# Optimization experiments

Hardware: AMD Instinct MI355X
Metric: run time of the kernel (lower is better)

Reference implementation:

```python
import math
import jax, jax.numpy as jnp
import numpy as np

NUM_HEADS, RAD_PTS, LVL_PTS = 8, 4, 1
P = RAD_PTS * LVL_PTS


def setup_inputs() -> dict:
    B, Nq, Din = 2, 21760, 256
    hw = np.array([[128, 128], [64, 64], [32, 32], [16, 16]], np.int64)
    sizes = hw[:, 0] * hw[:, 1]
    offs = np.concatenate([[0], np.cumsum(sizes)[:-1]]).astype(np.int64)
    Ns = int(sizes.sum())
    map_ids = np.tile(np.repeat(np.arange(4), sizes)[None], (B, 1)).astype(np.int64)

    key = jax.random.key(0)
    ks = jax.random.split(key, 8)
    in_feats = jax.random.normal(ks[0], (B, Nq, Din), jnp.float32)
    sample_feats = jax.random.normal(ks[1], (B, Ns, Din), jnp.float32)
    sample_priors = jax.random.uniform(ks[2], (B, Nq, 2), jnp.float32)

    # sample_offsets bias: radial grid init as in the torch module
    thetas = np.arange(NUM_HEADS) * (2.0 * math.pi / NUM_HEADS)
    grid = np.stack([np.cos(thetas), np.sin(thetas), np.zeros(NUM_HEADS)], 1)
    grid = grid / np.abs(grid).max(1, keepdims=True)
    grid = np.tile(grid.reshape(NUM_HEADS, 1, 1, 3), (1, RAD_PTS, LVL_PTS, 1))
    grid = grid * np.arange(1, RAD_PTS + 1).reshape(1, RAD_PTS, 1, 1)
    bo = jnp.asarray(grid.reshape(-1), jnp.float32)

    Wo = jax.random.normal(ks[3], (NUM_HEADS * P * 3, Din), jnp.float32) * 0.01
    Wa = jax.random.normal(ks[4], (NUM_HEADS * P, Din), jnp.float32) * 0.01
    ba = jnp.zeros((NUM_HEADS * P,), jnp.float32)
    s = 1.0 / np.sqrt(Din)
    Wv = jax.random.normal(ks[5], (Din, Din), jnp.float32) * s
    bv = jnp.zeros((Din,), jnp.float32)
    Wout = jax.random.normal(ks[6], (Din, Din), jnp.float32) * s
    bout = jnp.zeros((Din,), jnp.float32)

    return dict(in_feats=in_feats, sample_priors=sample_priors, sample_feats=sample_feats,
                map_hw=jnp.asarray(hw), map_offs=jnp.asarray(offs), map_ids=jnp.asarray(map_ids),
                Wo=Wo, bo=bo, Wa=Wa, ba=ba, Wv=Wv, bv=bv, Wout=Wout, bout=bout)


def _trilinear_sample(val, map_hw, map_offs, xy, z, L):
    # val [B,Ns,H,D]; xy [B,Q,H,P,2] normalized; z [B,Q,H,P] in ~[0,1]
    B, Ns, H, D = val.shape
    Q = xy.shape[1]
    val_t = val.transpose(0, 2, 1, 3)  # [B,H,Ns,D]
    x, y = xy[..., 0], xy[..., 1]
    lvl_f = z * (L - 1)
    l0 = jnp.floor(lvl_f).astype(jnp.int32)
    wz = lvl_f - l0.astype(lvl_f.dtype)

    def gather(idx):  # idx [B,Q,H,P] int32 -> [B,Q,H,P,D]
        it = idx.transpose(0, 2, 1, 3).reshape(B, H, Q * P, 1)
        g = jnp.take_along_axis(val_t, it, axis=2)  # [B,H,Q*P,D]
        return g.reshape(B, H, Q, P, D).transpose(0, 2, 1, 3, 4)

    def sample_level(lvl):  # bilinear sample within pyramid level `lvl` (zero padding)
        valid_l = (lvl >= 0) & (lvl < L)
        lc = jnp.clip(lvl, 0, L - 1)
        Hl = map_hw[lc, 0].astype(jnp.int32)
        Wl = map_hw[lc, 1].astype(jnp.int32)
        off = map_offs[lc].astype(jnp.int32)
        xf = x * Wl.astype(x.dtype) - 0.5
        yf = y * Hl.astype(x.dtype) - 0.5
        x0 = jnp.floor(xf).astype(jnp.int32)
        y0 = jnp.floor(yf).astype(jnp.int32)
        dx = xf - x0.astype(x.dtype)
        dy = yf - y0.astype(x.dtype)
        out = jnp.zeros((B, Q, H, P, D), x.dtype)
        corners = [(x0, y0, (1 - dx) * (1 - dy)), (x0 + 1, y0, dx * (1 - dy)),
                   (x0, y0 + 1, (1 - dx) * dy), (x0 + 1, y0 + 1, dx * dy)]
        for xi, yi, w in corners:
            ok = valid_l & (xi >= 0) & (xi < Wl) & (yi >= 0) & (yi < Hl)
            idx = off + jnp.clip(yi, 0, Hl - 1) * Wl + jnp.clip(xi, 0, Wl - 1)
            out = out + gather(idx) * (w * ok.astype(x.dtype))[..., None]
        return out

    return sample_level(l0) * (1 - wz)[..., None] + sample_level(l0 + 1) * wz[..., None]


def reference(in_feats, sample_priors, sample_feats, map_hw, map_offs, map_ids,
              Wo, bo, Wa, ba, Wv, bv, Wout, bout):
    B, Nq, _ = in_feats.shape
    Ns = sample_feats.shape[1]
    L = map_hw.shape[0]
    D = Wv.shape[0] // NUM_HEADS

    val = (sample_feats @ Wv.T + bv).reshape(B, Ns, NUM_HEADS, D)
    offs = (in_feats @ Wo.T + bo).reshape(B, Nq, NUM_HEADS, P, 3)

    # sample_priors last dim == 2: normalize offsets by (W, H) of the query's map
    norm = map_hw[:, ::-1][map_ids].astype(offs.dtype)  # [B,Nq,2] (w,h)
    sample_xy = sample_priors[:, :, None, None, :2] + offs[..., :2] / norm[:, :, None, None, :]

    lvl_off = jnp.arange(LVL_PTS, dtype=offs.dtype) - 0.5 * (LVL_PTS - 1)
    z_grid = map_ids[:, :, None, None, None].astype(offs.dtype) + lvl_off  # [B,Nq,1,1,Lp]
    z_grid = jnp.broadcast_to(z_grid, (B, Nq, NUM_HEADS, RAD_PTS, LVL_PTS)).reshape(B, Nq, NUM_HEADS, P)
    sample_z = (z_grid + jnp.tanh(offs[..., 2])) / (L - 1)

    attn = jax.nn.softmax((in_feats @ Wa.T + ba).reshape(B, Nq, NUM_HEADS, P), axis=3)

    sampled = _trilinear_sample(val, map_hw, map_offs, sample_xy, sample_z, L)  # [B,Nq,H,P,D]
    attn_feats = jnp.einsum('bqhpd,bqhp->bqhd', sampled, attn).reshape(B, Nq, NUM_HEADS * D)
    return attn_feats @ Wout.T + bout
```

## Files before the change

### kernel.cpp

```cpp
#include <hip/hip_runtime.h>
#include <hip/hip_bf16.h>
#include <math.h>

typedef __bf16 bf16x8 __attribute__((ext_vector_type(8)));
typedef float f32x4 __attribute__((ext_vector_type(4)));
typedef unsigned short ushort8 __attribute__((ext_vector_type(8)));

static __device__ __forceinline__ unsigned short f2bf(float f) {
    union { float f; unsigned u; } c; c.f = f;
    unsigned r = c.u + 0x7FFFu + ((c.u >> 16) & 1u);
    return (unsigned short)(r >> 16);
}
static __device__ __forceinline__ float bf2f(unsigned short u) {
    union { unsigned u; float f; } c; c.u = ((unsigned)u) << 16;
    return c.f;
}

__global__ __launch_bounds__(256) void convert_weights(
    const float* __restrict__ Wv, const float* __restrict__ Wo,
    const float* __restrict__ Wa, const float* __restrict__ Wout,
    const float* __restrict__ bo, const float* __restrict__ ba,
    unsigned short* __restrict__ Wv_b, unsigned short* __restrict__ Woa_b,
    unsigned short* __restrict__ Wout_b, float* __restrict__ boa)
{
    int gid = blockIdx.x * blockDim.x + threadIdx.x;
    int stride = gridDim.x * blockDim.x;
    for (int i = gid; i < 163840; i += stride) {
        if (i < 65536)       Wv_b[i] = f2bf(Wv[i]);
        else if (i < 90112)  Woa_b[i - 65536] = f2bf(Wo[i - 65536]);
        else if (i < 98304)  Woa_b[i - 65536] = f2bf(Wa[i - 90112]);
        else                 Wout_b[i - 98304] = f2bf(Wout[i - 98304]);
    }
    if (gid < 96)       boa[gid] = bo[gid];
    else if (gid < 128) boa[gid] = ba[gid - 96];
}

template<int WN, bool A_BF16, int OUT_MODE>
__global__ __launch_bounds__(WN * 64) void gemm_mfma(
    const void* __restrict__ Av, const unsigned short* __restrict__ W,
    const float* __restrict__ bias, void* __restrict__ Cv,
    int M, int N, int K, int NsPB)
{
    constexpr int BM = 64;
    constexpr int BN = WN * 64;
    constexpr int BK = 64;
    constexpr int NTHR = WN * 64;
    constexpr int LDP = 72;

    __shared__ __align__(16) unsigned short smem[(BM + BN) * LDP];
    unsigned short* As = smem;
    unsigned short* Bs = smem + BM * LDP;

    const int bm  = blockIdx.x * BM;
    const int bn  = blockIdx.y * BN;
    const int tid = threadIdx.x;
    const int wid = tid >> 6;
    const int lane = tid & 63;
    const int lr = lane & 15;
    const int lg = lane >> 4;

    f32x4 acc[4][4];
    #pragma unroll
    for (int mi = 0; mi < 4; ++mi)
        #pragma unroll
        for (int ni = 0; ni < 4; ++ni)
            acc[mi][ni] = (f32x4){0.f, 0.f, 0.f, 0.f};

    for (int kt = 0; kt < K; kt += BK) {
        if (A_BF16) {
            const unsigned short* A = (const unsigned short*)Av;
            #pragma unroll
            for (int u = tid; u < BM * 8; u += NTHR) {
                int r = u >> 3, kb = u & 7;
                ushort8 v = *(const ushort8*)(A + (size_t)(bm + r) * K + kt + kb * 8);
                *(ushort8*)(As + r * LDP + kb * 8) = v;
            }
        } else {
            const float* A = (const float*)Av;
            #pragma unroll
            for (int u = tid; u < BM * 8; u += NTHR) {
                int r = u >> 3, kb = u & 7;
                const float* src = A + (size_t)(bm + r) * K + kt + kb * 8;
                float4 f0 = *(const float4*)(src);
                float4 f1 = *(const float4*)(src + 4);
                ushort8 v;
                v[0] = f2bf(f0.x); v[1] = f2bf(f0.y);
                v[2] = f2bf(f0.z); v[3] = f2bf(f0.w);
                v[4] = f2bf(f1.x); v[5] = f2bf(f1.y);
                v[6] = f2bf(f1.z); v[7] = f2bf(f1.w);
                *(ushort8*)(As + r * LDP + kb * 8) = v;
            }
        }
        #pragma unroll
        for (int u = tid; u < BN * 8; u += NTHR) {
            int r = u >> 3, kb = u & 7;
            ushort8 v = *(const ushort8*)(W + (size_t)(bn + r) * K + kt + kb * 8);
            *(ushort8*)(Bs + r * LDP + kb * 8) = v;
        }
        __syncthreads();

        #pragma unroll
        for (int kk = 0; kk < 2; ++kk) {
            bf16x8 fa[4], fb[4];
            #pragma unroll
            for (int mi = 0; mi < 4; ++mi)
                fa[mi] = *(const bf16x8*)(As + (mi * 16 + lr) * LDP + kk * 32 + lg * 8);
            #pragma unroll
            for (int ni = 0; ni < 4; ++ni)
                fb[ni] = *(const bf16x8*)(Bs + (wid * 64 + ni * 16 + lr) * LDP + kk * 32 + lg * 8);
            #pragma unroll
            for (int mi = 0; mi < 4; ++mi)
                #pragma unroll
                for (int ni = 0; ni < 4; ++ni)
                    acc[mi][ni] = __builtin_amdgcn_mfma_f32_16x16x32_bf16(
                        fa[mi], fb[ni], acc[mi][ni], 0, 0, 0);
        }
        __syncthreads();
    }

    if (OUT_MODE == 2) {
        const int b = bm / NsPB;
        const int ns_base = bm - b * NsPB;
        #pragma unroll
        for (int ni = 0; ni < 4; ++ni) {
            int col = wid * 64 + ni * 16 + lr;
            int h   = col >> 5;
            int ch  = col & 31;
            float bv = bias[col];
            unsigned short* dst = (unsigned short*)Cv +
                (size_t)(b * 8 + h) * NsPB * 32 + ch;
            #pragma unroll
            for (int mi = 0; mi < 4; ++mi) {
                #pragma unroll
                for (int r = 0; r < 4; ++r) {
                    int ns = ns_base + mi * 16 + lg * 4 + r;
                    dst[(size_t)ns * 32] = f2bf(acc[mi][ni][r] + bv);
                }
            }
        }
    } else {
        #pragma unroll
        for (int ni = 0; ni < 4; ++ni) {
            int col = bn + wid * 64 + ni * 16 + lr;
            float bv = bias[col];
            #pragma unroll
            for (int mi = 0; mi < 4; ++mi) {
                #pragma unroll
                for (int r = 0; r < 4; ++r) {
                    int row = bm + mi * 16 + lg * 4 + r;
                    if (OUT_MODE == 1) {
                        ((unsigned short*)Cv)[(size_t)row * N + col] =
                            f2bf(acc[mi][ni][r] + bv);
                    } else {
                        ((float*)Cv)[(size_t)row * N + col] = acc[mi][ni][r] + bv;
                    }
                }
            }
        }
    }
}

__global__ __launch_bounds__(256) void msda_sample_kernel(
    const float* __restrict__ C1,
    const float* __restrict__ priors,
    const unsigned short* __restrict__ val,
    const int*   __restrict__ map_hw,
    const int*   __restrict__ map_offs,
    const int*   __restrict__ map_ids,
    unsigned short* __restrict__ out,
    int Nq, int Ns)
{
    const int swz = (blockIdx.x & 7) * (gridDim.x >> 3) + (blockIdx.x >> 3);
    const int qh  = threadIdx.x >> 7;
    const int bq  = swz * 2 + qh;
    const int t   = threadIdx.x & 127;
    const int b   = bq / Nq;
    const int q   = bq - b * Nq;

    __shared__ float s_w[2][32][9];
    __shared__ int   s_i[2][32][9];
    __shared__ float s_red[2][32][9];

    if (t < 32) {
        const int h = t >> 2;
        const int p = t & 3;
        const float* sc = C1 + (size_t)bq * 128;
        float o0 = sc[h * 12 + p * 3 + 0];
        float o1 = sc[h * 12 + p * 3 + 1];
        float o2 = sc[h * 12 + p * 3 + 2];
        float logit = sc[96 + h * 4 + p];

        float m = logit;
        m = fmaxf(m, __shfl_xor(m, 1));
        m = fmaxf(m, __shfl_xor(m, 2));
        float e = expf(logit - m);
        float s = e;
        s += __shfl_xor(s, 1);
        s += __shfl_xor(s, 2);
        float attnw = e / s;

        int lid = map_ids[(size_t)b * Ns + q];
        float px = priors[(size_t)bq * 2 + 0];
        float py = priors[(size_t)bq * 2 + 1];
        int Hq = map_hw[lid * 2 + 0];
        int Wq = map_hw[lid * 2 + 1];
        float x = px + o0 / (float)Wq;
        float y = py + o1 / (float)Hq;

        float lvl_f = (float)lid + tanhf(o2);
        float l0f = floorf(lvl_f);
        int   l0  = (int)l0f;
        float wz  = lvl_f - l0f;

        #pragma unroll
        for (int sl = 0; sl < 2; ++sl) {
            int   lv = l0 + sl;
            float wl = sl ? wz : (1.0f - wz);
            float w4[4];
            int   i4[4];
            if (lv >= 0 && lv < 4) {
                int Hs  = map_hw[lv * 2 + 0];
                int Ws  = map_hw[lv * 2 + 1];
                int off = map_offs[lv];
                float xf = x * (float)Ws - 0.5f;
                float yf = y * (float)Hs - 0.5f;
                float x0f = floorf(xf), y0f = floorf(yf);
                int   x0  = (int)x0f,  y0  = (int)y0f;
                float dx = xf - x0f, dy = yf - y0f;
                #pragma unroll
                for (int j = 0; j < 4; ++j) {
                    int xi = x0 + (j & 1);
                    int yi = y0 + (j >> 1);
                    float w = ((j & 1) ? dx : 1.0f - dx) *
                              ((j >> 1) ? dy : 1.0f - dy);
                    bool ok = (xi >= 0) && (xi < Ws) && (yi >= 0) && (yi < Hs);
                    w4[j] = ok ? (w * wl * attnw) : 0.0f;
                    i4[j] = ok ? ((off + yi * Ws + xi) << 5) : 0;
                }
            } else {
                #pragma unroll
                for (int j = 0; j < 4; ++j) { w4[j] = 0.0f; i4[j] = 0; }
            }
            #pragma unroll
            for (int j = 0; j < 4; ++j) {
                s_w[qh][t][sl * 4 + j] = w4[j];
                s_i[qh][t][sl * 4 + j] = i4[j];
            }
        }
    }
    __syncthreads();

    const int p  = t >> 5;
    const int s  = t & 31;
    const int h  = s >> 2;
    const int d8 = s & 3;
    const int hp = h * 4 + p;

    float w[8];
    int   ix[8];
    #pragma unroll
    for (int j = 0; j < 8; ++j) { w[j] = s_w[qh][hp][j]; ix[j] = s_i[qh][hp][j]; }

    const unsigned short* vb = val + (size_t)(b * 8 + h) * Ns * 32 + d8 * 8;
    float acc[8] = {0.f, 0.f, 0.f, 0.f, 0.f, 0.f, 0.f, 0.f};
    #pragma unroll
    for (int j = 0; j < 8; ++j) {
        ushort8 v = *(const ushort8*)(vb + (size_t)ix[j]);
        #pragma unroll
        for (int c = 0; c < 8; ++c)
            acc[c] += w[j] * bf2f(v[c]);
    }

    #pragma unroll
    for (int c = 0; c < 8; ++c)
        acc[c] += __shfl_xor(acc[c], 32);

    if (t >= 64 && t < 96) {
        #pragma unroll
        for (int c = 0; c < 8; ++c)
            s_red[qh][t - 64][c] = acc[c];
    }
    __syncthreads();

    if (t < 32) {
        ushort8 o;
        #pragma unroll
        for (int c = 0; c < 8; ++c)
            o[c] = f2bf(acc[c] + s_red[qh][t][c]);
        *(ushort8*)(out + (size_t)bq * 256 + t * 8) = o;
    }
}

extern "C" void kernel_launch(void* const* d_in, const int* in_sizes, int n_in,
                              void* d_out, int out_size, void* d_ws, size_t ws_size,
                              hipStream_t stream) {
    const float* in_feats      = (const float*)d_in[0];
    const float* sample_priors = (const float*)d_in[1];
    const float* sample_feats  = (const float*)d_in[2];
    const int*   map_hw        = (const int*)d_in[3];
    const int*   map_offs      = (const int*)d_in[4];
    const int*   map_ids       = (const int*)d_in[5];
    const float* Wo            = (const float*)d_in[6];
    const float* bo            = (const float*)d_in[7];
    const float* Wa            = (const float*)d_in[8];
    const float* ba            = (const float*)d_in[9];
    const float* Wv            = (const float*)d_in[10];
    const float* bv            = (const float*)d_in[11];
    const float* Wout          = (const float*)d_in[12];
    const float* bout          = (const float*)d_in[13];
    float* out = (float*)d_out;

    const int B = 2, Nq = 21760, Din = 256;
    const int Ns = in_sizes[2] / (B * Din);
    const int BQ = B * Nq;

    unsigned short* val = (unsigned short*)d_out;
    float* C1 = (float*)d_ws;
    unsigned short* af = (unsigned short*)((char*)d_ws + (size_t)BQ * 128 * 4);
    char* wbase = (char*)d_ws + (size_t)BQ * 128 * 4 + (size_t)BQ * 256 * 2;
    unsigned short* Wv_b   = (unsigned short*)wbase;
    unsigned short* Woa_b  = Wv_b + 65536;
    unsigned short* Wout_b = Woa_b + 32768;
    float* boa = (float*)(Wout_b + 65536);

    convert_weights<<<dim3(160), dim3(256), 0, stream>>>(
        Wv, Wo, Wa, Wout, bo, ba, Wv_b, Woa_b, Wout_b, boa);

    gemm_mfma<4, false, 2><<<dim3(BQ / 64, 1), dim3(256), 0, stream>>>(
        sample_feats, Wv_b, bv, val, B * Ns, 256, Din, Ns);

    gemm_mfma<2, false, 0><<<dim3(BQ / 64, 1), dim3(128), 0, stream>>>(
        in_feats, Woa_b, boa, C1, BQ, 128, Din, Ns);

    msda_sample_kernel<<<dim3(BQ / 2), dim3(256), 0, stream>>>(
        C1, sample_priors, val, map_hw, map_offs, map_ids, af, Nq, Ns);

    gemm_mfma<4, true, 0><<<dim3(BQ / 64, 1), dim3(256), 0, stream>>>(
        af, Wout_b, bout, out, BQ, 256, Din, Ns);
}
```

Baseline: 128.3 us.

## Reorder sampling queries by prior y-band for gather locality

Adds a histogram and scatter pass that buckets queries by batch and the y-coordinate band of their sample prior, then makes the sampling kernel process queries in that bucketed order. Neighbouring blocks then gather from nearby rows of the value maps, which should improve L2 cache reuse for the random-access bilinear gathers. In exchange it adds two small kernels, including a single-block histogram that serialises over all queries, plus an extra indirection load in the sampler. Writes to the output stay indexed by the original query, so results are unchanged.

```diff
diff --git a/kernel.cpp b/kernel.cpp
--- a/kernel.cpp
+++ b/kernel.cpp
@@ -33,6 +33,55 @@
     }
     if (gid < 96)       boa[gid] = bo[gid];
     else if (gid < 128) boa[gid] = ba[gid - 96];
+}
+
+__global__ __launch_bounds__(1024) void bucket_hist(
+    const float* __restrict__ priors, int* __restrict__ bws, int BQ, int Nq)
+{
+    __shared__ int cnt[16];
+    if (threadIdx.x < 16) cnt[threadIdx.x] = 0;
+    __syncthreads();
+    for (int q = threadIdx.x; q < BQ; q += 1024) {
+        int b = q / Nq;
+        float py = priors[(size_t)q * 2 + 1];
+        int band = min(7, max(0, (int)(py * 8.0f)));
+        atomicAdd(&cnt[b * 8 + band], 1);
+    }
+    __syncthreads();
+    if (threadIdx.x == 0) {
+        int acc = 0;
+        for (int i = 0; i < 16; ++i) {
+            int c = cnt[i];
+            bws[i] = acc;
+            bws[16 + i] = acc;
+            acc += c;
+        }
+    }
+}
+
+__global__ __launch_bounds__(256) void bucket_scatter(
+    const float* __restrict__ priors, int* __restrict__ bws,
+    int* __restrict__ qidx, int BQ, int Nq)
+{
+    __shared__ int lcnt[16];
+    __shared__ int lbase[16];
+    const int tid = threadIdx.x;
+    if (tid < 16) lcnt[tid] = 0;
+    __syncthreads();
+    int q = blockIdx.x * 256 + tid;
+    int mybucket = 0, myslot = 0;
+    bool valid = q < BQ;
+    if (valid) {
+        int b = q / Nq;
+        float py = priors[(size_t)q * 2 + 1];
+        int band = min(7, max(0, (int)(py * 8.0f)));
+        mybucket = b * 8 + band;
+        myslot = atomicAdd(&lcnt[mybucket], 1);
+    }
+    __syncthreads();
+    if (tid < 16) lbase[tid] = atomicAdd(&bws[16 + tid], lcnt[tid]);
+    __syncthreads();
+    if (valid) qidx[lbase[mybucket] + myslot] = q;
 }
 
 template<int WN, bool A_BF16, int OUT_MODE>
@@ -167,12 +216,13 @@
     const int*   __restrict__ map_hw,
     const int*   __restrict__ map_offs,
     const int*   __restrict__ map_ids,
+    const int*   __restrict__ qidx,
     unsigned short* __restrict__ out,
     int Nq, int Ns)
 {
     const int swz = (blockIdx.x & 7) * (gridDim.x >> 3) + (blockIdx.x >> 3);
     const int qh  = threadIdx.x >> 7;
-    const int bq  = swz * 2 + qh;
+    const int bq  = qidx[swz * 2 + qh];
     const int t   = threadIdx.x & 127;
     const int b   = bq / Nq;
     const int q   = bq - b * Nq;
@@ -322,10 +372,16 @@
     unsigned short* Woa_b  = Wv_b + 65536;
     unsigned short* Wout_b = Woa_b + 32768;
     float* boa = (float*)(Wout_b + 65536);
+    int* bws  = (int*)(boa + 128);
+    int* qidx = bws + 32;
 
     convert_weights<<<dim3(160), dim3(256), 0, stream>>>(
         Wv, Wo, Wa, Wout, bo, ba, Wv_b, Woa_b, Wout_b, boa);
 
+    bucket_hist<<<dim3(1), dim3(1024), 0, stream>>>(sample_priors, bws, BQ, Nq);
+    bucket_scatter<<<dim3((BQ + 255) / 256), dim3(256), 0, stream>>>(
+        sample_priors, bws, qidx, BQ, Nq);
+
     gemm_mfma<4, false, 2><<<dim3(BQ / 64, 1), dim3(256), 0, stream>>>(
         sample_feats, Wv_b, bv, val, B * Ns, 256, Din, Ns);
 
@@ -333,7 +389,7 @@
         in_feats, Woa_b, boa, C1, BQ, 128, Din, Ns);
 
     msda_sample_kernel<<<dim3(BQ / 2), dim3(256), 0, stream>>>(
-        C1, sample_priors, val, map_hw, map_offs, map_ids, af, Nq, Ns);
+        C1, sample_priors, val, map_hw, map_offs, map_ids, qidx, af, Nq, Ns);
 
     gemm_mfma<4, true, 0><<<dim3(BQ / 64, 1), dim3(256), 0, stream>>>(
         af, Wout_b, bout, out, BQ, 256, Din, Ns);
```

After: 142.4 us. 1.11x slower.
